# Kernel tuning notes

Measured on AMD Instinct MI355X. Metric: run time of the kernel, lower is better.

## Reference

```python
import jax, jax.numpy as jnp
import numpy as np

HARD_DIST_CUTOFF = 2.0  # init kwarg of ExternalNeighbors


def setup_inputs() -> dict:
    key = jax.random.key(0)
    ks = jax.random.split(key, 6)
    n_mol, n_atoms = 128, 1024
    n_real = n_mol * n_atoms          # 131072
    n_pairs = 8388608                 # ~64 neighbors per atom
    coordinates = jax.random.normal(ks[0], (n_mol, n_atoms, 3), dtype=jnp.float32)
    real_atoms = jax.random.randint(ks[1], (n_real,), 0, n_mol * n_atoms, dtype=jnp.int64)
    shifts = jax.random.randint(ks[2], (n_pairs, 3), 0, 2, dtype=jnp.int32)
    cell = jax.random.normal(ks[3], (3, 3), dtype=jnp.float32)
    pair_first = jax.random.randint(ks[4], (n_pairs,), 0, n_real, dtype=jnp.int64)
    pair_second = jax.random.randint(ks[5], (n_pairs,), 0, n_real, dtype=jnp.int64)
    return {"coordinates": coordinates, "real_atoms": real_atoms, "shifts": shifts,
            "cell": cell, "pair_first": pair_first, "pair_second": pair_second}


def reference(coordinates, real_atoms, shifts, cell, pair_first, pair_second):
    n_mol, n_atoms, _ = coordinates.shape
    # gather real-atom coordinates from flattened (mol*atom, 3)
    atom_coordinates = coordinates.reshape(n_mol * n_atoms, 3)[real_atoms]
    # pair displacement with periodic shift: [n_pairs, 3]
    paircoord = (atom_coordinates[pair_second] - atom_coordinates[pair_first]
                 + shifts.astype(cell.dtype) @ cell)
    distflat = jnp.linalg.norm(paircoord, axis=1)  # [n_pairs]
    # torch version does boolean compaction (dynamic shape); in jax we keep
    # fixed shape and zero/mask-out pairs beyond the cutoff, returning the mask.
    mask = distflat < HARD_DIST_CUTOFF
    distflat_m = jnp.where(mask, distflat, 0.0)
    pair_first_m = jnp.where(mask, pair_first, -1)
    pair_second_m = jnp.where(mask, pair_second, -1)
    paircoord_m = jnp.where(mask[:, None], paircoord, 0.0)
    return distflat_m, pair_first_m, pair_second_m, paircoord_m, mask
```

## Files before the change

### kernel.cpp

```cpp
#include <hip/hip_runtime.h>


#define HARD_DIST_CUTOFF 2.0f

__global__ __launch_bounds__(256) void external_neighbors_v2(
    const float* __restrict__ coords,
    const int*   __restrict__ real_atoms,
    const int*   __restrict__ shifts,
    const float* __restrict__ cell,
    const int*   __restrict__ pair_first,
    const int*   __restrict__ pair_second,
    float* __restrict__ out,
    int n_pairs)
{
    const float c00 = cell[0], c01 = cell[1], c02 = cell[2];
    const float c10 = cell[3], c11 = cell[4], c12 = cell[5];
    const float c20 = cell[6], c21 = cell[7], c22 = cell[8];

    const size_t N = (size_t)n_pairs;
    float* __restrict__ out_dist = out;
    float* __restrict__ out_pf   = out + N;
    float* __restrict__ out_ps   = out + 2 * N;
    float* __restrict__ out_pc   = out + 3 * N;
    float* __restrict__ out_mask = out + 6 * N;

    const int tid  = blockIdx.x * blockDim.x + threadIdx.x;
    const int base = tid * 4;

    if (base + 3 < n_pairs) {
        const int4 pf4 = *reinterpret_cast<const int4*>(pair_first  + base);
        const int4 ps4 = *reinterpret_cast<const int4*>(pair_second + base);
        const int4* sh = reinterpret_cast<const int4*>(shifts + 3 * base);
        const int4 sA = sh[0], sB = sh[1], sC = sh[2];

        const int pf[4] = {pf4.x, pf4.y, pf4.z, pf4.w};
        const int ps[4] = {ps4.x, ps4.y, ps4.z, ps4.w};
        const int s0[4] = {sA.x, sA.w, sB.z, sC.y};
        const int s1[4] = {sA.y, sB.x, sB.w, sC.z};
        const int s2[4] = {sA.z, sB.y, sC.x, sC.w};

        int ia[4], ib[4];
        #pragma unroll
        for (int k = 0; k < 4; ++k) ia[k] = real_atoms[pf[k]];
        #pragma unroll
        for (int k = 0; k < 4; ++k) ib[k] = real_atoms[ps[k]];

        float ax[4], ay[4], az[4], bx[4], by[4], bz[4];
        #pragma unroll
        for (int k = 0; k < 4; ++k) {
            const float* ca = coords + 3 * (size_t)ia[k];
            ax[k] = ca[0]; ay[k] = ca[1]; az[k] = ca[2];
        }
        #pragma unroll
        for (int k = 0; k < 4; ++k) {
            const float* cb = coords + 3 * (size_t)ib[k];
            bx[k] = cb[0]; by[k] = cb[1]; bz[k] = cb[2];
        }

        float4 dist, pfo, pso, msk;
        float dxv[4], dyv[4], dzv[4];
        float* distp = &dist.x; float* pfp = &pfo.x;
        float* psp = &pso.x;   float* mkp = &msk.x;
        #pragma unroll
        for (int k = 0; k < 4; ++k) {
            const float f0 = (float)s0[k], f1 = (float)s1[k], f2 = (float)s2[k];
            const float dx = bx[k] - ax[k] + f0 * c00 + f1 * c10 + f2 * c20;
            const float dy = by[k] - ay[k] + f0 * c01 + f1 * c11 + f2 * c21;
            const float dz = bz[k] - az[k] + f0 * c02 + f1 * c12 + f2 * c22;
            const float d  = sqrtf(dx * dx + dy * dy + dz * dz);
            const bool  m  = d < HARD_DIST_CUTOFF;
            distp[k] = m ? d : 0.0f;
            pfp[k]   = m ? (float)pf[k] : -1.0f;
            psp[k]   = m ? (float)ps[k] : -1.0f;
            mkp[k]   = m ? 1.0f : 0.0f;
            dxv[k]   = m ? dx : 0.0f;
            dyv[k]   = m ? dy : 0.0f;
            dzv[k]   = m ? dz : 0.0f;
        }

        *reinterpret_cast<float4*>(out_dist + base) = dist;
        *reinterpret_cast<float4*>(out_pf   + base) = pfo;
        *reinterpret_cast<float4*>(out_ps   + base) = pso;
        *reinterpret_cast<float4*>(out_mask + base) = msk;
        float4* pc = reinterpret_cast<float4*>(out_pc + 3 * (size_t)base);
        pc[0] = make_float4(dxv[0], dyv[0], dzv[0], dxv[1]);
        pc[1] = make_float4(dyv[1], dzv[1], dxv[2], dyv[2]);
        pc[2] = make_float4(dzv[2], dxv[3], dyv[3], dzv[3]);
    } else {
        for (int p = base; p < n_pairs; ++p) {
            const int pfs = pair_first[p];
            const int pss = pair_second[p];
            const int t0 = shifts[3 * p + 0];
            const int t1 = shifts[3 * p + 1];
            const int t2 = shifts[3 * p + 2];
            const int iaa = real_atoms[pfs];
            const int ibb = real_atoms[pss];
            const float f0 = (float)t0, f1 = (float)t1, f2 = (float)t2;
            const float dx = coords[3*ibb+0] - coords[3*iaa+0] + f0*c00 + f1*c10 + f2*c20;
            const float dy = coords[3*ibb+1] - coords[3*iaa+1] + f0*c01 + f1*c11 + f2*c21;
            const float dz = coords[3*ibb+2] - coords[3*iaa+2] + f0*c02 + f1*c12 + f2*c22;
            const float d  = sqrtf(dx*dx + dy*dy + dz*dz);
            const bool  m  = d < HARD_DIST_CUTOFF;
            out_dist[p] = m ? d : 0.0f;
            out_pf[p]   = m ? (float)pfs : -1.0f;
            out_ps[p]   = m ? (float)pss : -1.0f;
            out_pc[3*(size_t)p+0] = m ? dx : 0.0f;
            out_pc[3*(size_t)p+1] = m ? dy : 0.0f;
            out_pc[3*(size_t)p+2] = m ? dz : 0.0f;
            out_mask[p] = m ? 1.0f : 0.0f;
        }
    }
}

extern "C" void kernel_launch(void* const* d_in, const int* in_sizes, int n_in,
                              void* d_out, int out_size, void* d_ws, size_t ws_size,
                              hipStream_t stream) {
    const float* coords      = (const float*)d_in[0];
    const int*   real_atoms  = (const int*)d_in[1];
    const int*   shifts      = (const int*)d_in[2];
    const float* cell        = (const float*)d_in[3];
    const int*   pair_first  = (const int*)d_in[4];
    const int*   pair_second = (const int*)d_in[5];
    float*       out         = (float*)d_out;

    const int n_pairs = in_sizes[4];

    const int block = 256;
    const int pairs_per_thread = 4;
    const int grid = (n_pairs + block * pairs_per_thread - 1) / (block * pairs_per_thread);

    external_neighbors_v2<<<grid, block, 0, stream>>>(
        coords, real_atoms, shifts, cell, pair_first, pair_second, out, n_pairs);
}
```

Baseline: 481.0 us.

## Precompute float4 gathered coordinate table to collapse double indirection

Adds a pre-pass kernel that resolves real_atoms indirection once per atom into a padded float4 table in workspace. The main kernel then does a single 16-byte gather per pair endpoint instead of an index load followed by three scalar coordinate loads. This removes a dependent random-access level and cuts gather transactions, at the cost of an extra small launch and a 2 MB table. A grid-stride fallback kernel is kept for when the workspace is too small.

```diff
diff --git a/kernel.cpp b/kernel.cpp
--- a/kernel.cpp
+++ b/kernel.cpp
@@ -3,13 +3,26 @@
 
 #define HARD_DIST_CUTOFF 2.0f
 
-__global__ __launch_bounds__(256) void external_neighbors_v2(
+__global__ __launch_bounds__(256) void build_gather_table(
     const float* __restrict__ coords,
     const int*   __restrict__ real_atoms,
-    const int*   __restrict__ shifts,
-    const float* __restrict__ cell,
-    const int*   __restrict__ pair_first,
-    const int*   __restrict__ pair_second,
+    float4* __restrict__ tab,
+    int n_real)
+{
+    const int i = blockIdx.x * blockDim.x + threadIdx.x;
+    if (i < n_real) {
+        const int a = real_atoms[i];
+        const float* c = coords + 3 * (size_t)a;
+        tab[i] = make_float4(c[0], c[1], c[2], 0.0f);
+    }
+}
+
+__global__ __launch_bounds__(256) void external_neighbors_v3(
+    const float4* __restrict__ tab,
+    const int*    __restrict__ shifts,
+    const float*  __restrict__ cell,
+    const int*    __restrict__ pair_first,
+    const int*    __restrict__ pair_second,
     float* __restrict__ out,
     int n_pairs)
 {
@@ -39,23 +52,11 @@
         const int s1[4] = {sA.y, sB.x, sB.w, sC.z};
         const int s2[4] = {sA.z, sB.y, sC.x, sC.w};
 
-        int ia[4], ib[4];
+        float4 A[4], B[4];
         #pragma unroll
-        for (int k = 0; k < 4; ++k) ia[k] = real_atoms[pf[k]];
+        for (int k = 0; k < 4; ++k) A[k] = tab[pf[k]];
         #pragma unroll
-        for (int k = 0; k < 4; ++k) ib[k] = real_atoms[ps[k]];
-
-        float ax[4], ay[4], az[4], bx[4], by[4], bz[4];
-        #pragma unroll
-        for (int k = 0; k < 4; ++k) {
-            const float* ca = coords + 3 * (size_t)ia[k];
-            ax[k] = ca[0]; ay[k] = ca[1]; az[k] = ca[2];
-        }
-        #pragma unroll
-        for (int k = 0; k < 4; ++k) {
-            const float* cb = coords + 3 * (size_t)ib[k];
-            bx[k] = cb[0]; by[k] = cb[1]; bz[k] = cb[2];
-        }
+        for (int k = 0; k < 4; ++k) B[k] = tab[ps[k]];
 
         float4 dist, pfo, pso, msk;
         float dxv[4], dyv[4], dzv[4];
@@ -64,9 +65,9 @@
         #pragma unroll
         for (int k = 0; k < 4; ++k) {
             const float f0 = (float)s0[k], f1 = (float)s1[k], f2 = (float)s2[k];
-            const float dx = bx[k] - ax[k] + f0 * c00 + f1 * c10 + f2 * c20;
-            const float dy = by[k] - ay[k] + f0 * c01 + f1 * c11 + f2 * c21;
-            const float dz = bz[k] - az[k] + f0 * c02 + f1 * c12 + f2 * c22;
+            const float dx = B[k].x - A[k].x + f0 * c00 + f1 * c10 + f2 * c20;
+            const float dy = B[k].y - A[k].y + f0 * c01 + f1 * c11 + f2 * c21;
+            const float dz = B[k].z - A[k].z + f0 * c02 + f1 * c12 + f2 * c22;
             const float d  = sqrtf(dx * dx + dy * dy + dz * dz);
             const bool  m  = d < HARD_DIST_CUTOFF;
             distp[k] = m ? d : 0.0f;
@@ -90,16 +91,15 @@
         for (int p = base; p < n_pairs; ++p) {
             const int pfs = pair_first[p];
             const int pss = pair_second[p];
-            const int t0 = shifts[3 * p + 0];
-            const int t1 = shifts[3 * p + 1];
-            const int t2 = shifts[3 * p + 2];
-            const int iaa = real_atoms[pfs];
-            const int ibb = real_atoms[pss];
-            const float f0 = (float)t0, f1 = (float)t1, f2 = (float)t2;
-            const float dx = coords[3*ibb+0] - coords[3*iaa+0] + f0*c00 + f1*c10 + f2*c20;
-            const float dy = coords[3*ibb+1] - coords[3*iaa+1] + f0*c01 + f1*c11 + f2*c21;
-            const float dz = coords[3*ibb+2] - coords[3*iaa+2] + f0*c02 + f1*c12 + f2*c22;
-            const float d  = sqrtf(dx*dx + dy*dy + dz*dz);
+            const float f0 = (float)shifts[3 * p + 0];
+            const float f1 = (float)shifts[3 * p + 1];
+            const float f2 = (float)shifts[3 * p + 2];
+            const float4 Aa = tab[pfs];
+            const float4 Bb = tab[pss];
+            const float dx = Bb.x - Aa.x + f0 * c00 + f1 * c10 + f2 * c20;
+            const float dy = Bb.y - Aa.y + f0 * c01 + f1 * c11 + f2 * c21;
+            const float dz = Bb.z - Aa.z + f0 * c02 + f1 * c12 + f2 * c22;
+            const float d  = sqrtf(dx * dx + dy * dy + dz * dz);
             const bool  m  = d < HARD_DIST_CUTOFF;
             out_dist[p] = m ? d : 0.0f;
             out_pf[p]   = m ? (float)pfs : -1.0f;
@@ -109,6 +109,50 @@
             out_pc[3*(size_t)p+2] = m ? dz : 0.0f;
             out_mask[p] = m ? 1.0f : 0.0f;
         }
+    }
+}
+
+__global__ __launch_bounds__(256) void external_neighbors_v2(
+    const float* __restrict__ coords,
+    const int*   __restrict__ real_atoms,
+    const int*   __restrict__ shifts,
+    const float* __restrict__ cell,
+    const int*   __restrict__ pair_first,
+    const int*   __restrict__ pair_second,
+    float* __restrict__ out,
+    int n_pairs)
+{
+    const float c00 = cell[0], c01 = cell[1], c02 = cell[2];
+    const float c10 = cell[3], c11 = cell[4], c12 = cell[5];
+    const float c20 = cell[6], c21 = cell[7], c22 = cell[8];
+    const size_t N = (size_t)n_pairs;
+    float* out_dist = out;
+    float* out_pf   = out + N;
+    float* out_ps   = out + 2 * N;
+    float* out_pc   = out + 3 * N;
+    float* out_mask = out + 6 * N;
+    const int tid = blockIdx.x * blockDim.x + threadIdx.x;
+    const int stride = gridDim.x * blockDim.x;
+    for (int p = tid; p < n_pairs; p += stride) {
+        const int pfs = pair_first[p];
+        const int pss = pair_second[p];
+        const float f0 = (float)shifts[3 * p + 0];
+        const float f1 = (float)shifts[3 * p + 1];
+        const float f2 = (float)shifts[3 * p + 2];
+        const int iaa = real_atoms[pfs];
+        const int ibb = real_atoms[pss];
+        const float dx = coords[3*ibb+0] - coords[3*iaa+0] + f0*c00 + f1*c10 + f2*c20;
+        const float dy = coords[3*ibb+1] - coords[3*iaa+1] + f0*c01 + f1*c11 + f2*c21;
+        const float dz = coords[3*ibb+2] - coords[3*iaa+2] + f0*c02 + f1*c12 + f2*c22;
+        const float d  = sqrtf(dx*dx + dy*dy + dz*dz);
+        const bool  m  = d < HARD_DIST_CUTOFF;
+        out_dist[p] = m ? d : 0.0f;
+        out_pf[p]   = m ? (float)pfs : -1.0f;
+        out_ps[p]   = m ? (float)pss : -1.0f;
+        out_pc[3*(size_t)p+0] = m ? dx : 0.0f;
+        out_pc[3*(size_t)p+1] = m ? dy : 0.0f;
+        out_pc[3*(size_t)p+2] = m ? dz : 0.0f;
+        out_mask[p] = m ? 1.0f : 0.0f;
     }
 }
 
@@ -123,12 +167,22 @@
     const int*   pair_second = (const int*)d_in[5];
     float*       out         = (float*)d_out;
 
+    const int n_real  = in_sizes[1];
     const int n_pairs = in_sizes[4];
 
-    const int block = 256;
-    const int pairs_per_thread = 4;
-    const int grid = (n_pairs + block * pairs_per_thread - 1) / (block * pairs_per_thread);
+    const size_t tab_bytes = (size_t)n_real * sizeof(float4);
 
-    external_neighbors_v2<<<grid, block, 0, stream>>>(
-        coords, real_atoms, shifts, cell, pair_first, pair_second, out, n_pairs);
+    if (ws_size >= tab_bytes) {
+        float4* tab = (float4*)d_ws;
+        build_gather_table<<<(n_real + 255) / 256, 256, 0, stream>>>(
+            coords, real_atoms, tab, n_real);
+
+        const int block = 256;
+        const int grid  = (n_pairs + block * 4 - 1) / (block * 4);
+        external_neighbors_v3<<<grid, block, 0, stream>>>(
+            tab, shifts, cell, pair_first, pair_second, out, n_pairs);
+    } else {
+        external_neighbors_v2<<<2048, 256, 0, stream>>>(
+            coords, real_atoms, shifts, cell, pair_first, pair_second, out, n_pairs);
+    }
 }
```

Measured after the change: 440.0 us. 1.09x faster.
